# Kernel tuning notes

Measured on AMD Instinct MI355X. Metric: run time of the kernel, lower is better.

Reference implementation:

```python
import jax, jax.numpy as jnp
import numpy as np

P, Q, R = 3, 1, 0
N_GEN = P + Q + R        # number of basis vectors
DIM = 2 ** N_GEN         # 16 blades


def _build_cayley(p, q, r):
    """Dense sign tensor T[i, j, c] = sign of e_i * e_j = sign * e_c."""
    n = p + q + r
    D = 2 ** n
    metric = np.zeros(n)
    metric[:p] = 1.0
    metric[p:p + q] = -1.0

    def blade_sign(a_idx, b_idx):
        a_bits = [i for i in range(n) if (a_idx >> i) & 1]
        b_bits = [i for i in range(n) if (b_idx >> i) & 1]
        sign = 1.0
        result = list(a_bits)
        for b in b_bits:
            pos = len(result)
            swaps = 0
            for i in range(len(result) - 1, -1, -1):
                if result[i] < b:
                    break
                if result[i] == b:
                    sign *= float(metric[b])
                    sign *= (-1.0) ** swaps
                    result.pop(i)
                    pos = -1
                    break
                swaps += 1
            if pos != -1:
                sign *= (-1.0) ** swaps
                result.insert(pos - swaps, b)
        c = sum(1 << bit for bit in result)
        return sign, c

    T = np.zeros((D, D, D), dtype=np.float32)
    for i in range(D):
        for j in range(D):
            s, c = blade_sign(i, j)
            T[i, j, c] = s
    return T


CAYLEY = jnp.asarray(_build_cayley(P, Q, R))  # [16, 16, 16] constant


def setup_inputs() -> dict:
    key = jax.random.key(0)
    ka, kb = jax.random.split(key)
    N = 1048576
    a = jax.random.normal(ka, (N, DIM), dtype=jnp.float32)
    b = jax.random.normal(kb, (N, DIM), dtype=jnp.float32)
    return {"a": a, "b": b}


def reference(a, b):
    # (a x b)_c = sum_{i,j} sign(i,j,c) * a_i * b_j  -- sparse bilinear
    # contraction through the precomputed Cayley table.
    out = jnp.einsum("ni,nj,ijc->nc", a, b, CAYLEY)
    out = jnp.nan_to_num(out, nan=0.0, posinf=10000.0, neginf=-10000.0)
    out = jnp.clip(out, -1000.0, 1000.0)
    return out
```

## Files before the change

### kernel.cpp

```cpp
#include <hip/hip_runtime.h>


typedef float vfloat4 __attribute__((ext_vector_type(4)));

struct CayleyTab { signed char s[16][16]; };

constexpr CayleyTab build_tab() {
    CayleyTab t{};
    for (int i = 0; i < 16; ++i) {
        for (int j = 0; j < 16; ++j) {
            int sum = 0;
            for (int a = i >> 1; a; a >>= 1) {
                int m = a & j;
                while (m) { sum += (m & 1); m >>= 1; }
            }
            sum += ((i & j) >> 3) & 1;
            t.s[i][j] = (signed char)((sum & 1) ? -1 : 1);
        }
    }
    return t;
}

constexpr CayleyTab TAB = build_tab();

__device__ __forceinline__ float clip1000(float v) {
    return fminf(fmaxf(v, -1000.0f), 1000.0f);
}

#define ROW_STRIDE 68

__global__ __launch_bounds__(128) void clifford_gp_kernel(
        const float* __restrict__ a,
        const float* __restrict__ b,
        float* __restrict__ out,
        int nrows) {
    __shared__ float lds[2][64 * ROW_STRIDE];

    const int wid  = threadIdx.x >> 6;
    const int lane = threadIdx.x & 63;
    float* buf = lds[wid];

    const int R0 = blockIdx.x * 128 + wid * 64;
    if (R0 >= nrows) return;
    const size_t gbase = (size_t)R0 * 16;

    const int wrow = lane >> 2;
    const int wq   = (lane & 3) * 4;

    vfloat4 pa[4], pb[4];
    #pragma unroll
    for (int k = 0; k < 4; ++k) {
        pa[k] = *reinterpret_cast<const vfloat4*>(a + gbase + (size_t)(k * 64 + lane) * 4);
        pb[k] = *reinterpret_cast<const vfloat4*>(b + gbase + (size_t)(k * 64 + lane) * 4);
    }

    float av[16], bv[16];

    #pragma unroll
    for (int k = 0; k < 4; ++k)
        *reinterpret_cast<vfloat4*>(&buf[(16 * k + wrow) * ROW_STRIDE + wq]) = pa[k];
    #pragma unroll
    for (int qq = 0; qq < 4; ++qq) {
        const vfloat4 t = *reinterpret_cast<const vfloat4*>(&buf[lane * ROW_STRIDE + qq * 4]);
        av[4 * qq + 0] = t.x; av[4 * qq + 1] = t.y;
        av[4 * qq + 2] = t.z; av[4 * qq + 3] = t.w;
    }

    #pragma unroll
    for (int k = 0; k < 4; ++k)
        *reinterpret_cast<vfloat4*>(&buf[(16 * k + wrow) * ROW_STRIDE + wq]) = pb[k];
    #pragma unroll
    for (int qq = 0; qq < 4; ++qq) {
        const vfloat4 t = *reinterpret_cast<const vfloat4*>(&buf[lane * ROW_STRIDE + qq * 4]);
        bv[4 * qq + 0] = t.x; bv[4 * qq + 1] = t.y;
        bv[4 * qq + 2] = t.z; bv[4 * qq + 3] = t.w;
    }

    float acc[16];
    #pragma unroll
    for (int c = 0; c < 16; ++c) acc[c] = 0.0f;
    #pragma unroll
    for (int i = 0; i < 16; ++i) {
        #pragma unroll
        for (int j = 0; j < 16; ++j) {
            const int c = i ^ j;
            if (TAB.s[i][j] > 0) acc[c] = fmaf(av[i],  bv[j], acc[c]);
            else                 acc[c] = fmaf(av[i], -bv[j], acc[c]);
        }
    }

    #pragma unroll
    for (int qq = 0; qq < 4; ++qq) {
        vfloat4 t;
        t.x = clip1000(acc[4 * qq + 0]);
        t.y = clip1000(acc[4 * qq + 1]);
        t.z = clip1000(acc[4 * qq + 2]);
        t.w = clip1000(acc[4 * qq + 3]);
        *reinterpret_cast<vfloat4*>(&buf[lane * ROW_STRIDE + qq * 4]) = t;
    }
    #pragma unroll
    for (int k = 0; k < 4; ++k) {
        const vfloat4 t = *reinterpret_cast<const vfloat4*>(&buf[(16 * k + wrow) * ROW_STRIDE + wq]);
        *reinterpret_cast<vfloat4*>(out + gbase + (size_t)(k * 64 + lane) * 4) = t;
    }
}

extern "C" void kernel_launch(void* const* d_in, const int* in_sizes, int n_in,
                              void* d_out, int out_size, void* d_ws, size_t ws_size,
                              hipStream_t stream) {
    const float* a = (const float*)d_in[0];
    const float* b = (const float*)d_in[1];
    float* out = (float*)d_out;

    const int nrows = in_sizes[0] / 16;
    const int block = 128;
    const int blocks = (nrows + 127) / 128;

    clifford_gp_kernel<<<blocks, block, 0, stream>>>(a, b, out, nrows);
}
```

Before: 34.19 us.

## Process two row tiles per wave with XOR-swizzled unpadded LDS transpose

```diff
diff --git a/kernel.cpp b/kernel.cpp
--- a/kernel.cpp
+++ b/kernel.cpp
@@ -27,81 +27,92 @@
     return fminf(fmaxf(v, -1000.0f), 1000.0f);
 }
 
-#define ROW_STRIDE 68
-
 __global__ __launch_bounds__(128) void clifford_gp_kernel(
         const float* __restrict__ a,
         const float* __restrict__ b,
         float* __restrict__ out,
         int nrows) {
-    __shared__ float lds[2][64 * ROW_STRIDE];
+    __shared__ float lds[2][64 * 16];
 
     const int wid  = threadIdx.x >> 6;
     const int lane = threadIdx.x & 63;
     float* buf = lds[wid];
 
-    const int R0 = blockIdx.x * 128 + wid * 64;
+    const int R0 = (blockIdx.x * 2 + wid) * 128;
     if (R0 >= nrows) return;
-    const size_t gbase = (size_t)R0 * 16;
 
-    const int wrow = lane >> 2;
-    const int wq   = (lane & 3) * 4;
+    const int w = lane >> 2;
+    const int q = lane & 3;
+    const int sW = (q + w + (w >> 2)) & 3;
+    int sR[4];
+    #pragma unroll
+    for (int qq = 0; qq < 4; ++qq)
+        sR[qq] = (qq + lane + (lane >> 2)) & 3;
 
-    vfloat4 pa[4], pb[4];
+    vfloat4 pa[2][4], pb[2][4];
     #pragma unroll
-    for (int k = 0; k < 4; ++k) {
-        pa[k] = *reinterpret_cast<const vfloat4*>(a + gbase + (size_t)(k * 64 + lane) * 4);
-        pb[k] = *reinterpret_cast<const vfloat4*>(b + gbase + (size_t)(k * 64 + lane) * 4);
-    }
-
-    float av[16], bv[16];
-
-    #pragma unroll
-    for (int k = 0; k < 4; ++k)
-        *reinterpret_cast<vfloat4*>(&buf[(16 * k + wrow) * ROW_STRIDE + wq]) = pa[k];
-    #pragma unroll
-    for (int qq = 0; qq < 4; ++qq) {
-        const vfloat4 t = *reinterpret_cast<const vfloat4*>(&buf[lane * ROW_STRIDE + qq * 4]);
-        av[4 * qq + 0] = t.x; av[4 * qq + 1] = t.y;
-        av[4 * qq + 2] = t.z; av[4 * qq + 3] = t.w;
-    }
-
-    #pragma unroll
-    for (int k = 0; k < 4; ++k)
-        *reinterpret_cast<vfloat4*>(&buf[(16 * k + wrow) * ROW_STRIDE + wq]) = pb[k];
-    #pragma unroll
-    for (int qq = 0; qq < 4; ++qq) {
-        const vfloat4 t = *reinterpret_cast<const vfloat4*>(&buf[lane * ROW_STRIDE + qq * 4]);
-        bv[4 * qq + 0] = t.x; bv[4 * qq + 1] = t.y;
-        bv[4 * qq + 2] = t.z; bv[4 * qq + 3] = t.w;
-    }
-
-    float acc[16];
-    #pragma unroll
-    for (int c = 0; c < 16; ++c) acc[c] = 0.0f;
-    #pragma unroll
-    for (int i = 0; i < 16; ++i) {
+    for (int t = 0; t < 2; ++t) {
+        const size_t gb = (size_t)(R0 + 64 * t) * 16;
         #pragma unroll
-        for (int j = 0; j < 16; ++j) {
-            const int c = i ^ j;
-            if (TAB.s[i][j] > 0) acc[c] = fmaf(av[i],  bv[j], acc[c]);
-            else                 acc[c] = fmaf(av[i], -bv[j], acc[c]);
+        for (int k = 0; k < 4; ++k) {
+            pa[t][k] = *reinterpret_cast<const vfloat4*>(a + gb + (size_t)(k * 64 + lane) * 4);
+            pb[t][k] = *reinterpret_cast<const vfloat4*>(b + gb + (size_t)(k * 64 + lane) * 4);
         }
     }
 
     #pragma unroll
-    for (int qq = 0; qq < 4; ++qq) {
-        vfloat4 t;
-        t.x = clip1000(acc[4 * qq + 0]);
-        t.y = clip1000(acc[4 * qq + 1]);
-        t.z = clip1000(acc[4 * qq + 2]);
-        t.w = clip1000(acc[4 * qq + 3]);
-        *reinterpret_cast<vfloat4*>(&buf[lane * ROW_STRIDE + qq * 4]) = t;
-    }
-    #pragma unroll
-    for (int k = 0; k < 4; ++k) {
-        const vfloat4 t = *reinterpret_cast<const vfloat4*>(&buf[(16 * k + wrow) * ROW_STRIDE + wq]);
-        *reinterpret_cast<vfloat4*>(out + gbase + (size_t)(k * 64 + lane) * 4) = t;
+    for (int t = 0; t < 2; ++t) {
+        const size_t gb = (size_t)(R0 + 64 * t) * 16;
+
+        float av[16], bv[16];
+
+        #pragma unroll
+        for (int k = 0; k < 4; ++k)
+            *reinterpret_cast<vfloat4*>(&buf[(16 * k + w) * 16 + sW * 4]) = pa[t][k];
+        #pragma unroll
+        for (int qq = 0; qq < 4; ++qq) {
+            const vfloat4 v = *reinterpret_cast<const vfloat4*>(&buf[lane * 16 + sR[qq] * 4]);
+            av[4 * qq + 0] = v.x; av[4 * qq + 1] = v.y;
+            av[4 * qq + 2] = v.z; av[4 * qq + 3] = v.w;
+        }
+
+        #pragma unroll
+        for (int k = 0; k < 4; ++k)
+            *reinterpret_cast<vfloat4*>(&buf[(16 * k + w) * 16 + sW * 4]) = pb[t][k];
+        #pragma unroll
+        for (int qq = 0; qq < 4; ++qq) {
+            const vfloat4 v = *reinterpret_cast<const vfloat4*>(&buf[lane * 16 + sR[qq] * 4]);
+            bv[4 * qq + 0] = v.x; bv[4 * qq + 1] = v.y;
+            bv[4 * qq + 2] = v.z; bv[4 * qq + 3] = v.w;
+        }
+
+        float acc[16];
+        #pragma unroll
+        for (int c = 0; c < 16; ++c) acc[c] = 0.0f;
+        #pragma unroll
+        for (int i = 0; i < 16; ++i) {
+            #pragma unroll
+            for (int j = 0; j < 16; ++j) {
+                const int c = i ^ j;
+                if (TAB.s[i][j] > 0) acc[c] = fmaf(av[i],  bv[j], acc[c]);
+                else                 acc[c] = fmaf(av[i], -bv[j], acc[c]);
+            }
+        }
+
+        #pragma unroll
+        for (int qq = 0; qq < 4; ++qq) {
+            vfloat4 v;
+            v.x = clip1000(acc[4 * qq + 0]);
+            v.y = clip1000(acc[4 * qq + 1]);
+            v.z = clip1000(acc[4 * qq + 2]);
+            v.w = clip1000(acc[4 * qq + 3]);
+            *reinterpret_cast<vfloat4*>(&buf[lane * 16 + sR[qq] * 4]) = v;
+        }
+        #pragma unroll
+        for (int k = 0; k < 4; ++k) {
+            const vfloat4 v = *reinterpret_cast<const vfloat4*>(&buf[(16 * k + w) * 16 + sW * 4]);
+            *reinterpret_cast<vfloat4*>(out + gb + (size_t)(k * 64 + lane) * 4) = v;
+        }
     }
 }
 
@@ -114,7 +125,7 @@
 
     const int nrows = in_sizes[0] / 16;
     const int block = 128;
-    const int blocks = (nrows + 127) / 128;
+    const int blocks = (nrows + 255) / 256;
 
     clifford_gp_kernel<<<blocks, block, 0, stream>>>(a, b, out, nrows);
 }
```

Result: no change. 34.63 us (+1.3%).
